# Kernel optimization log

Measured on AMD Instinct MI355X. Metric: run time of the kernel, lower is better.

Reference implementation:

```python
import jax, jax.numpy as jnp
import numpy as np

B, S, E, H, FFN = 4, 1024, 1024, 16, 4096
D = E // H
EPS = 1e-5


def setup_inputs() -> dict:
    key = jax.random.key(0)
    ks = jax.random.split(key, 13)
    n = lambda k, shp, sc=1.0: jax.random.normal(k, shp, jnp.float32) * sc
    return {
        "x": n(ks[0], (B, S, E)),
        "wq": n(ks[1], (E, E), E ** -0.5),
        "wk": n(ks[2], (E, E), E ** -0.5),
        "wv": n(ks[3], (E, E), E ** -0.5),
        "phase": n(ks[4], (H, D)),  # nn.Parameter(torch.randn(H, d_k))
        "ln1_g": jnp.ones((E,), jnp.float32),
        "ln1_b": jnp.zeros((E,), jnp.float32),
        "ln2_g": jnp.ones((E,), jnp.float32),
        "ln2_b": jnp.zeros((E,), jnp.float32),
        "w1": n(ks[5], (FFN, E), E ** -0.5),
        "b1": n(ks[6], (FFN,), 0.02),
        "w2": n(ks[7], (E, FFN), FFN ** -0.5),
        "b2": n(ks[8], (E,), 0.02),
    }


def _layer_norm(x, g, b):
    mu = jnp.mean(x, -1, keepdims=True)
    xc = x - mu
    var = jnp.mean(xc * xc, -1, keepdims=True)  # biased, like torch LayerNorm
    return xc * jax.lax.rsqrt(var + EPS) * g + b


def reference(x, wq, wk, wv, phase, ln1_g, ln1_b, ln2_g, ln2_b, w1, b1, w2, b2):
    b_, s_, e_ = x.shape

    def proj(w):  # torch Linear: x @ w.T, then split heads -> [B,H,S,D]
        return jnp.einsum("bse,fe->bsf", x, w).reshape(b_, s_, H, D).transpose(0, 2, 1, 3)

    q, k, v = proj(wq), proj(wk), proj(wv)
    ph = jnp.exp(1j * phase)[None, :, None, :]  # [1,H,1,D] complex64
    qc, kc, vc = q * ph, k * ph, v * ph
    # complex QK^T (note: plain transpose, NOT conjugate, per source)
    scores = jnp.einsum("bhsd,bhtd->bhst", qc, kc) / jnp.sqrt(jnp.float32(D))
    # complex softmax: exp(z)/sum exp(z), stabilized by max of real part
    m = jnp.max(scores.real, -1, keepdims=True)
    ez = jnp.exp(scores - m)
    attn = ez / jnp.sum(ez, -1, keepdims=True)
    out = jnp.einsum("bhst,bhtd->bhsd", attn, vc).real  # take real part to re-enter real pipeline
    out = out.transpose(0, 2, 1, 3).reshape(b_, s_, e_)
    x1 = _layer_norm(x + out, ln1_g, ln1_b)
    h = jax.nn.relu(jnp.einsum("bse,fe->bsf", x1, w1) + b1)
    ffn = jnp.einsum("bsf,ef->bse", h, w2) + b2
    return _layer_norm(x1 + ffn, ln2_g, ln2_b)
```

## Files before the change

kernel.cpp:

```cpp
#include <hip/hip_runtime.h>

typedef unsigned short u16;
typedef unsigned int u32;
typedef u16 u16x4 __attribute__((ext_vector_type(4)));
typedef u16 u16x8 __attribute__((ext_vector_type(8)));
typedef u32 u32x2 __attribute__((ext_vector_type(2)));
typedef u32 u32x4 __attribute__((ext_vector_type(4)));
typedef float f32x4 __attribute__((ext_vector_type(4)));
typedef __bf16 bf16x8 __attribute__((ext_vector_type(8)));

#define B_N 4
#define S_N 1024
#define E_N 1024
#define H_N 16
#define D_N 64
#define F_N 4096
#define NTOK 4096

#define SCK 0.18033688011112042f
#define SSK 0.01989436788648692f

static __device__ __forceinline__ u16 f2bf(float f) {
  u32 u = __builtin_bit_cast(u32, f);
  return (u16)((u + 0x7fffu + ((u >> 16) & 1u)) >> 16);
}
static __device__ __forceinline__ float bf2f(u16 v) {
  return __builtin_bit_cast(float, ((u32)v) << 16);
}
static __device__ __forceinline__ f32x4 mfma16(u16x8 a, u16x8 b, f32x4 c) {
  return __builtin_amdgcn_mfma_f32_16x16x32_bf16(
      __builtin_bit_cast(bf16x8, a), __builtin_bit_cast(bf16x8, b), c, 0, 0, 0);
}
static __device__ __forceinline__ float exp2_hw(float x) {
  float r; asm("v_exp_f32 %0, %1" : "=v"(r) : "v"(x)); return r;
}
static __device__ __forceinline__ float sin_hw(float x) {
  float r; asm("v_sin_f32 %0, %1" : "=v"(r) : "v"(x)); return r;
}
static __device__ __forceinline__ float cos_hw(float x) {
  float r; asm("v_cos_f32 %0, %1" : "=v"(r) : "v"(x)); return r;
}
static __device__ __forceinline__ u32 cvtpk(float lo, float hi) {
  u32 r; asm("v_cvt_pk_bf16_f32 %0, %1, %2" : "=v"(r) : "v"(lo), "v"(hi)); return r;
}
#define GLOAD16(gp, lp)                                              \
  __builtin_amdgcn_global_load_lds(                                  \
      (const __attribute__((address_space(1))) void*)(gp),           \
      (__attribute__((address_space(3))) void*)(lp), 16, 0, 0)

__global__ __launch_bounds__(256) void cvt_all(
    const float* __restrict__ s0, u16* __restrict__ d0, int n0,
    const float* __restrict__ s1, u16* __restrict__ d1, int n1,
    const float* __restrict__ s2, u16* __restrict__ d2, int n2,
    const float* __restrict__ s3, u16* __restrict__ d3, int n3,
    const float* __restrict__ s4, u16* __restrict__ d4, int n4,
    const float* __restrict__ s5, u16* __restrict__ d5, int n5) {
  const int seg = blockIdx.y;
  const float* src; u16* dst; int n;
  switch (seg) {
    case 0: src = s0; dst = d0; n = n0; break;
    case 1: src = s1; dst = d1; n = n1; break;
    case 2: src = s2; dst = d2; n = n2; break;
    case 3: src = s3; dst = d3; n = n3; break;
    case 4: src = s4; dst = d4; n = n4; break;
    default: src = s5; dst = d5; n = n5; break;
  }
  int i = blockIdx.x * 256 + threadIdx.x;
  if (i < n) {
    float4 v = ((const float4*)src)[i];
    u16x4 o;
    o[0] = f2bf(v.x); o[1] = f2bf(v.y); o[2] = f2bf(v.z); o[3] = f2bf(v.w);
    ((u16x4*)dst)[i] = o;
  }
}

template <int MODE, int KTILES>
__global__ __launch_bounds__(512, 4) void gemm2p(
    const u16* __restrict__ A, const u16* __restrict__ B0,
    const u16* __restrict__ B1, const u16* __restrict__ B2, int strideK,
    u16* __restrict__ o0, u16* __restrict__ o1, u16* __restrict__ o2,
    const float* __restrict__ biasp) {
  constexpr int BM = 128, BN = 128;
  constexpr int MR = BM / 32;
  constexpr int NR = BN / 64;
  constexpr int CA = BM / 64;
  constexpr int CB = BN / 64;
  constexpr int RS = BN * 2;
  constexpr int CM = BN / 8 - 1;
  constexpr int LCPR = 4;
  constexpr int RC = (BM * BN) / 4096;
  __shared__ u16 SMEM[(BM + BN) * 128];
  char* const base = (char*)SMEM;
  auto Abase = [&](int b) { return base + b * (BM * 128); };
  auto Bbase = [&](int b) { return base + 2 * (BM * 128) + b * (BN * 128); };

  const int tid = threadIdx.x;
  const int lane = tid & 63, wv = tid >> 6;
  const int l15 = lane & 15, l4 = lane >> 4;
  const int wr = wv >> 2, wc = wv & 3;

  int lin = blockIdx.x;
  { const int q = (int)gridDim.x >> 3; lin = (lin & 7) * q + (lin >> 3); }
  int bxr, by, kc = 0, region = 0;
  const u16* Bsrc = B0;
  if constexpr (MODE == 0) {
    const int bxa = lin % 24; by = lin / 24;
    region = bxa >> 3; bxr = bxa & 7;
    Bsrc = (region == 0) ? B0 : (region == 1) ? B1 : B2;
  } else if constexpr (MODE == 1) {
    bxr = lin & 31; by = lin >> 5;
  } else {
    bxr = lin & 7; by = (lin >> 3) & 31; kc = lin >> 8;
  }

  const u16* Ab = A + (size_t)(by * BM) * strideK + (size_t)kc * (KTILES * 64);
  const u16* Bb = Bsrc + (size_t)(bxr * BN) * strideK + (size_t)kc * (KTILES * 64);

  auto stage = [&](int buf, int kt) {
#pragma unroll
    for (int i = 0; i < CA; ++i) {
      const int c = (wv * CA + i) * 64 + lane;
      const int row = c >> 3, slot = (c & 7) ^ (row & 7);
      GLOAD16(Ab + (size_t)row * strideK + kt * 64 + slot * 8,
              Abase(buf) + (wv * CA + i) * 1024);
    }
#pragma unroll
    for (int i = 0; i < CB; ++i) {
      const int c = (wv * CB + i) * 64 + lane;
      const int row = c >> 3, slot = (c & 7) ^ (row & 7);
      GLOAD16(Bb + (size_t)row * strideK + kt * 64 + slot * 8,
              Bbase(buf) + (wv * CB + i) * 1024);
    }
  };

  f32x4 z4 = {0.f, 0.f, 0.f, 0.f};
  f32x4 acc[MR][NR];
#pragma unroll
  for (int m = 0; m < MR; ++m)
#pragma unroll
    for (int n = 0; n < NR; ++n) acc[m][n] = z4;

  stage(0, 0);
  __syncthreads();

  int buf = 0;
#pragma unroll 1
  for (int t = 0; t < KTILES; ++t) {
    if (t + 1 < KTILES) stage(buf ^ 1, t + 1);
#pragma unroll
    for (int kp = 0; kp < 2; ++kp) {
      u16x8 afr[MR], bfr[NR];
#pragma unroll
      for (int m = 0; m < MR; ++m) {
        const int row = wr * (BM / 2) + m * 16 + l15;
        const int off = row * 128 + ((((kp << 2) | l4) ^ (row & 7)) << 4);
        afr[m] = *(const u16x8*)(Abase(buf) + off);
      }
#pragma unroll
      for (int n = 0; n < NR; ++n) {
        const int row = wc * (BN / 4) + n * 16 + l15;
        const int off = row * 128 + ((((kp << 2) | l4) ^ (row & 7)) << 4);
        bfr[n] = *(const u16x8*)(Bbase(buf) + off);
      }
      __builtin_amdgcn_s_setprio(1);
#pragma unroll
      for (int m = 0; m < MR; ++m)
#pragma unroll
        for (int n = 0; n < NR; ++n) acc[m][n] = mfma16(afr[m], bfr[n], acc[m][n]);
      __builtin_amdgcn_s_setprio(0);
    }
    if (t + 1 < KTILES) {
      __syncthreads();
      buf ^= 1;
    }
  }

  __syncthreads();
  float bvv[NR];
  if constexpr (MODE == 1) {
#pragma unroll
    for (int n = 0; n < NR; ++n)
      bvv[n] = biasp[bxr * BN + wc * (BN / 4) + n * 16 + l15];
  }
  const bool vtile = (MODE == 0) && (region == 2);
#pragma unroll
  for (int n = 0; n < NR; ++n)
#pragma unroll
    for (int m = 0; m < MR; ++m)
#pragma unroll
      for (int j = 0; j < 4; ++j) {
        const int row = wr * (BM / 2) + m * 16 + l4 * 4 + j;
        const int col = wc * (BN / 4) + n * 16 + l15;
        float v = acc[m][n][j];
        if constexpr (MODE == 1) v = fmaxf(v + bvv[n], 0.f);
        const int fr = vtile ? col : row;
        const int fc = vtile ? row : col;
        *(u16*)(base + fr * RS + ((((fc >> 3) ^ (fr & CM))) << 4) +
                (fc & 7) * 2) = f2bf(v);
      }
  __syncthreads();
  if constexpr (MODE == 0) {
    if (region == 2) {
#pragma unroll
      for (int i = 0; i < RC; ++i) {
        const int q = i * 512 + tid;
        const int crow = q >> LCPR, slot = q & CM;
        const u16x8 v = *(const u16x8*)(base + crow * RS +
                                        ((slot ^ (crow & CM)) << 4));
        const int ch = bxr * BN + crow;
        const int hI = ch >> 6, dI = ch & 63;
        const int tok = by * BM + slot * 8;
        const int bI = tok >> 10, sI = tok & 1023;
        *(u16x8*)(o2 + (((size_t)(bI * H_N + hI)) * D_N + dI) * S_N + sI) = v;
      }
    } else {
      u16* outb = (region == 0) ? o0 : o1;
#pragma unroll
      for (int i = 0; i < RC; ++i) {
        const int q = i * 512 + tid;
        const int row = q >> LCPR, c = q & CM;
        const u16x8 v = *(const u16x8*)(base + row * RS +
                                        ((c ^ (row & CM)) << 4));
        const int gr = by * BM + row;
        const int gcol = bxr * BN + c * 8;
        const int bI = gr >> 10, sI = gr & 1023;
        const int hI = gcol >> 6, dI = gcol & 63;
        *(u16x8*)(outb + (((size_t)(bI * H_N + hI)) * S_N + sI) * D_N + dI) = v;
      }
    }
  } else if constexpr (MODE == 1) {
#pragma unroll
    for (int i = 0; i < RC; ++i) {
      const int q = i * 512 + tid;
      const int row = q >> LCPR, c = q & CM;
      const u16x8 v = *(const u16x8*)(base + row * RS + ((c ^ (row & CM)) << 4));
      *(u16x8*)(o0 + (size_t)(by * BM + row) * F_N + bxr * BN + c * 8) = v;
    }
  } else {
#pragma unroll
    for (int i = 0; i < RC; ++i) {
      const int q = i * 512 + tid;
      const int row = q >> LCPR, c = q & CM;
      const u16x8 v = *(const u16x8*)(base + row * RS + ((c ^ (row & CM)) << 4));
      const size_t gr = (size_t)kc * NTOK + by * BM + row;
      *(u16x8*)(o0 + gr * E_N + bxr * BN + c * 8) = v;
    }
  }
}

__global__ __launch_bounds__(512, 4) void attn_kernel(
    const u16* __restrict__ Qg, const u16* __restrict__ Kg,
    const u16* __restrict__ Vtg, const float* __restrict__ phase,
    u16* __restrict__ outp) {
  __shared__ u16 KS[64 * 64];
  __shared__ u16 VT[64 * 64];
  __shared__ u16 PreS[128 * 32], PimS[128 * 32];

  const int tid = threadIdx.x;
  const int lane = tid & 63, wv = tid >> 6;
  const int l15 = lane & 15, l4 = lane >> 4;
  const int L = blockIdx.x;
  const int within = L >> 3;
  const int qt = within & 7;
  const int g = (L & 7) * 8 + (within >> 3);
  const int hh = g & 15, bb = g >> 4;
  const size_t hoff = ((size_t)(bb * H_N + hh)) * (size_t)(S_N * D_N);
  const u16* K0 = Kg + hoff;
  const u16* Vt0 = Vtg + hoff;
  const int qrow = wv * 16 + l15;

  u16x8 qcf[2], qsf[2];
#pragma unroll
  for (int ks = 0; ks < 2; ++ks) {
    const u16x8 qraw = *(const u16x8*)(
        Qg + hoff + (size_t)(qt * 128 + qrow) * D_N + ks * 32 + l4 * 8);
#pragma unroll
    for (int e = 0; e < 8; ++e) {
      const int d = ks * 32 + l4 * 8 + e;
      float sp, cp;
      __sincosf(2.f * phase[hh * 64 + d], &sp, &cp);
      const float qv = bf2f(qraw[e]);
      qcf[ks][e] = f2bf(qv * cp * SCK);
      qsf[ks][e] = f2bf(qv * sp * SSK);
    }
  }

  f32x4 z4 = {0.f, 0.f, 0.f, 0.f};
  f32x4 U1[4], U2[4];
#pragma unroll
  for (int db = 0; db < 4; ++db) { U1[db] = z4; U2[db] = z4; }
  float zre = 0.f, zim = 0.f;

  const int krow = tid >> 3, kslot = tid & 7;
  const int loff = (krow * 128 + kslot * 16) ^ ((krow & 7) << 4);

  u32x4 rk = *(const u32x4*)(K0 + (size_t)krow * 64 + kslot * 8);
  u32x4 rv = *(const u32x4*)(Vt0 + (size_t)krow * S_N + kslot * 8);

  for (int kt = 0; kt < 16; ++kt) {
    *(u32x4*)((char*)KS + loff) = rk;
    *(u32x4*)((char*)VT + loff) = rv;
    if (kt < 15) {
      rk = *(const u32x4*)(K0 + (size_t)((kt + 1) * 64 + krow) * 64 + kslot * 8);
      rv = *(const u32x4*)(Vt0 + (size_t)krow * S_N + (kt + 1) * 64 + kslot * 8);
    }
    __syncthreads();

#pragma unroll
    for (int ts = 0; ts < 2; ++ts) {
      f32x4 sre[2], sim[2];
      sre[0] = z4; sre[1] = z4; sim[0] = z4; sim[1] = z4;
      __builtin_amdgcn_s_setprio(1);
#pragma unroll
      for (int tb = 0; tb < 2; ++tb) {
        const int trow = ts * 32 + tb * 16 + l15;
#pragma unroll
        for (int ks = 0; ks < 2; ++ks) {
          const int off = trow * 128 + ((((ks << 2) | l4) ^ (trow & 7)) << 4);
          u16x8 ak = *(const u16x8*)((const char*)KS + off);
          sre[tb] = mfma16(ak, qcf[ks], sre[tb]);
          sim[tb] = mfma16(ak, qsf[ks], sim[tb]);
        }
      }
      __builtin_amdgcn_s_setprio(0);

#pragma unroll
      for (int tb = 0; tb < 2; ++tb) {
        float pc[4], ps[4];
#pragma unroll
        for (int j = 0; j < 4; ++j) {
          const float e = exp2_hw(sre[tb][j]);
          const float sn = sin_hw(sim[tb][j]);
          const float cs = cos_hw(sim[tb][j]);
          pc[j] = e * cs; ps[j] = e * sn;
        }
        zre += (pc[0] + pc[1]) + (pc[2] + pc[3]);
        zim += (ps[0] + ps[1]) + (ps[2] + ps[3]);
        u32x2 wre = {cvtpk(pc[0], pc[1]), cvtpk(pc[2], pc[3])};
        u32x2 wim = {cvtpk(ps[0], ps[1]), cvtpk(ps[2], ps[3])};
        const int offp = (qrow * 64 + tb * 32 + l4 * 8) ^ (((qrow >> 1) & 3) << 4);
        *(u32x2*)((char*)PreS + offp) = wre;
        *(u32x2*)((char*)PimS + offp) = wim;
      }

      const int offp2 = (qrow * 64 + (l4 << 4)) ^ (((qrow >> 1) & 3) << 4);
      u16x8 bre = *(const u16x8*)((const char*)PreS + offp2);
      u16x8 bim = *(const u16x8*)((const char*)PimS + offp2);
      __builtin_amdgcn_s_setprio(1);
#pragma unroll
      for (int db = 0; db < 4; ++db) {
        const int dd = db * 16 + l15;
        const int offv = dd * 128 + ((((ts << 2) | l4) ^ (dd & 7)) << 4);
        u16x8 av = *(const u16x8*)((const char*)VT + offv);
        U1[db] = mfma16(av, bre, U1[db]);
        U2[db] = mfma16(av, bim, U2[db]);
      }
      __builtin_amdgcn_s_setprio(0);
    }
    __syncthreads();
  }

  float zr = zre, zi = zim;
  zr += __shfl_xor(zr, 16); zr += __shfl_xor(zr, 32);
  zi += __shfl_xor(zi, 16); zi += __shfl_xor(zi, 32);
  const float inv = 1.f / (zr * zr + zi * zi);
  const int q = qt * 128 + qrow;
  u16* orow = outp + ((size_t)(bb * S_N + q)) * E_N + hh * 64;
#pragma unroll
  for (int db = 0; db < 4; ++db) {
    float o[4];
#pragma unroll
    for (int j = 0; j < 4; ++j) {
      const int d = db * 16 + l4 * 4 + j;
      float sp, cp;
      __sincosf(phase[hh * 64 + d], &sp, &cp);
      const float nre = cp * U1[db][j] - sp * U2[db][j];
      const float nim = sp * U1[db][j] + cp * U2[db][j];
      o[j] = (nre * zr + nim * zi) * inv;
    }
    u32x2 w = {cvtpk(o[0], o[1]), cvtpk(o[2], o[3])};
    *(u32x2*)(orow + db * 16 + l4 * 4) = w;
  }
}

__global__ __launch_bounds__(256) void add_ln_kernel(
    const float* __restrict__ a, const u16* __restrict__ r,
    const float* __restrict__ g, const float* __restrict__ be,
    u16* __restrict__ outb) {
  const int tid = threadIdx.x;
  const int row = blockIdx.x;
  const int lane = tid & 63, wv = tid >> 6;
  const float4 va = ((const float4*)(a + (size_t)row * 1024))[tid];
  const u16x4 rr = *(const u16x4*)(r + (size_t)row * 1024 + tid * 4);
  float4 v;
  v.x = va.x + bf2f(rr[0]); v.y = va.y + bf2f(rr[1]);
  v.z = va.z + bf2f(rr[2]); v.w = va.w + bf2f(rr[3]);
  float s = v.x + v.y + v.z + v.w;
#pragma unroll
  for (int m = 1; m < 64; m <<= 1) s += __shfl_xor(s, m);
  __shared__ float red[8];
  if (lane == 0) red[wv] = s;
  __syncthreads();
  s = red[0] + red[1] + red[2] + red[3];
  const float mu = s * (1.f / 1024.f);
  float4 xc;
  xc.x = v.x - mu; xc.y = v.y - mu; xc.z = v.z - mu; xc.w = v.w - mu;
  float q = xc.x * xc.x + xc.y * xc.y + xc.z * xc.z + xc.w * xc.w;
#pragma unroll
  for (int m = 1; m < 64; m <<= 1) q += __shfl_xor(q, m);
  if (lane == 0) red[4 + wv] = q;
  __syncthreads();
  q = red[4] + red[5] + red[6] + red[7];
  const float rs = rsqrtf(q * (1.f / 1024.f) + 1e-5f);
  const float4 gg = ((const float4*)g)[tid];
  const float4 bb4 = ((const float4*)be)[tid];
  u16x4 ob;
  ob[0] = f2bf(xc.x * rs * gg.x + bb4.x);
  ob[1] = f2bf(xc.y * rs * gg.y + bb4.y);
  ob[2] = f2bf(xc.z * rs * gg.z + bb4.z);
  ob[3] = f2bf(xc.w * rs * gg.w + bb4.w);
  *(u16x4*)(outb + (size_t)row * 1024 + tid * 4) = ob;
}

__global__ __launch_bounds__(256) void add_ln4_kernel(
    const u16* __restrict__ part,
    const u16* __restrict__ resid,
    const float* __restrict__ bias,
    const float* __restrict__ g, const float* __restrict__ be,
    float* __restrict__ outp) {
  const int tid = threadIdx.x;
  const int row = blockIdx.x;
  const int lane = tid & 63, wv = tid >> 6;
  const float4 bv = ((const float4*)bias)[tid];
  float4 v = {bv.x, bv.y, bv.z, bv.w};
#pragma unroll
  for (int kc = 0; kc < 2; ++kc) {
    const u16x4 pp = *(const u16x4*)(part + ((size_t)kc * NTOK + row) * 1024 + tid * 4);
    v.x += bf2f(pp[0]); v.y += bf2f(pp[1]); v.z += bf2f(pp[2]); v.w += bf2f(pp[3]);
  }
  const u16x4 rr = *(const u16x4*)(resid + (size_t)row * 1024 + tid * 4);
  v.x += bf2f(rr[0]); v.y += bf2f(rr[1]); v.z += bf2f(rr[2]); v.w += bf2f(rr[3]);
  float s = v.x + v.y + v.z + v.w;
#pragma unroll
  for (int m = 1; m < 64; m <<= 1) s += __shfl_xor(s, m);
  __shared__ float red[8];
  if (lane == 0) red[wv] = s;
  __syncthreads();
  s = red[0] + red[1] + red[2] + red[3];
  const float mu = s * (1.f / 1024.f);
  float4 xc;
  xc.x = v.x - mu; xc.y = v.y - mu; xc.z = v.z - mu; xc.w = v.w - mu;
  float q = xc.x * xc.x + xc.y * xc.y + xc.z * xc.z + xc.w * xc.w;
#pragma unroll
  for (int m = 1; m < 64; m <<= 1) q += __shfl_xor(q, m);
  if (lane == 0) red[4 + wv] = q;
  __syncthreads();
  q = red[4] + red[5] + red[6] + red[7];
  const float rs = rsqrtf(q * (1.f / 1024.f) + 1e-5f);
  const float4 gg = ((const float4*)g)[tid];
  const float4 bb4 = ((const float4*)be)[tid];
  float4 o;
  o.x = xc.x * rs * gg.x + bb4.x;
  o.y = xc.y * rs * gg.y + bb4.y;
  o.z = xc.z * rs * gg.z + bb4.z;
  o.w = xc.w * rs * gg.w + bb4.w;
  ((float4*)(outp + (size_t)row * 1024))[tid] = o;
}

extern "C" void kernel_launch(void* const* d_in, const int* in_sizes, int n_in,
                              void* d_out, int out_size, void* d_ws, size_t ws_size,
                              hipStream_t stream) {
  (void)in_sizes; (void)n_in; (void)out_size; (void)ws_size;
  const float* x = (const float*)d_in[0];
  const float* wq = (const float*)d_in[1];
  const float* wk = (const float*)d_in[2];
  const float* wvp = (const float*)d_in[3];
  const float* phase = (const float*)d_in[4];
  const float* ln1g = (const float*)d_in[5];
  const float* ln1b = (const float*)d_in[6];
  const float* ln2g = (const float*)d_in[7];
  const float* ln2b = (const float*)d_in[8];
  const float* w1 = (const float*)d_in[9];
  const float* b1 = (const float*)d_in[10];
  const float* w2 = (const float*)d_in[11];
  const float* b2 = (const float*)d_in[12];
  float* outp = (float*)d_out;

  char* p = (char*)d_ws;
  auto alloc = [&](size_t n) -> char* {
    char* q = p;
    p += (n + 255) & ~(size_t)255;
    return q;
  };
  const size_t TOKE = (size_t)NTOK * E_N;
  u16* xb = (u16*)alloc(TOKE * 2);
  u16* wqb = (u16*)alloc((size_t)E_N * E_N * 2);
  u16* wkb = (u16*)alloc((size_t)E_N * E_N * 2);
  u16* wvb = (u16*)alloc((size_t)E_N * E_N * 2);
  u16* w1b = (u16*)alloc((size_t)F_N * E_N * 2);
  u16* w2b = (u16*)alloc((size_t)E_N * F_N * 2);
  u16* Qp  = (u16*)alloc(TOKE * 2);
  u16* pad = (u16*)alloc(TOKE * 2);
  u16* Kp  = (u16*)alloc(TOKE * 2);
  u16* Vtp = (u16*)alloc(TOKE * 2);
  u16* sp0 = (u16*)alloc(TOKE * 2);
  u16* attn_o = (u16*)alloc(TOKE * 4);
  alloc(TOKE * 2);
  (void)pad;
  u16* x1b = xb;
  u16* hb = Qp;
  u16* part = sp0;

  dim3 blk(256);
  cvt_all<<<dim3(4096, 6), blk, 0, stream>>>(
      x, xb, (int)(TOKE / 4),
      wq, wqb, E_N * E_N / 4,
      wk, wkb, E_N * E_N / 4,
      wvp, wvb, E_N * E_N / 4,
      w1, w1b, F_N * E_N / 4,
      w2, w2b, E_N * F_N / 4);

  gemm2p<0, 16><<<dim3(768), dim3(512), 0, stream>>>(
      xb, wqb, wkb, wvb, E_N, Qp, Kp, Vtp, nullptr);

  attn_kernel<<<dim3(512), dim3(512), 0, stream>>>(
      Qp, Kp, Vtp, phase, attn_o);

  add_ln_kernel<<<dim3(NTOK), blk, 0, stream>>>(x, attn_o, ln1g, ln1b, x1b);

  gemm2p<1, 16><<<dim3(1024), dim3(512), 0, stream>>>(
      x1b, w1b, nullptr, nullptr, E_N, hb, nullptr, nullptr, b1);

  gemm2p<2, 32><<<dim3(512), dim3(512), 0, stream>>>(
      hb, w2b, nullptr, nullptr, F_N, part, nullptr, nullptr, nullptr);

  add_ln4_kernel<<<dim3(NTOK), blk, 0, stream>>>(part, x1b, b2, ln2g, ln2b, outp);
}
```

Measured before the change: 178.5 us.

## Split attention key loop across two wave groups with LDS reduction

The attention kernel now launches 1024 threads per block as two groups of eight waves. Each group processes half of the key/value tiles in its own LDS buffers, and the partial accumulators and normalizer sums are then reduced through shared memory before group 0 writes the output. The aim is to double the waves resident per CU and halve the serial key-loop length, to better hide latency. The cost is a 64KB LDS footprint, an extra reduction epilogue, and tighter register limits from the new launch bounds, which could cause spilling.

```diff
diff --git a/kernel.cpp b/kernel.cpp
--- a/kernel.cpp
+++ b/kernel.cpp
@@ -248,17 +248,23 @@
   }
 }
 
-__global__ __launch_bounds__(512, 4) void attn_kernel(
+__global__ __launch_bounds__(1024, 8) void attn_kernel(
     const u16* __restrict__ Qg, const u16* __restrict__ Kg,
     const u16* __restrict__ Vtg, const float* __restrict__ phase,
     u16* __restrict__ outp) {
-  __shared__ u16 KS[64 * 64];
-  __shared__ u16 VT[64 * 64];
-  __shared__ u16 PreS[128 * 32], PimS[128 * 32];
+  __shared__ u16 SMEM[32768];
+  char* const base = (char*)SMEM;
 
   const int tid = threadIdx.x;
   const int lane = tid & 63, wv = tid >> 6;
+  const int grp = wv >> 3, wg = wv & 7;
+  const int tid_g = tid & 511;
   const int l15 = lane & 15, l4 = lane >> 4;
+  char* const KSb = base + grp * 8192;
+  char* const VTb = base + 16384 + grp * 8192;
+  char* const Preb = base + 32768 + grp * 8192;
+  char* const Pimb = base + 49152 + grp * 8192;
+
   const int L = blockIdx.x;
   const int within = L >> 3;
   const int qt = within & 7;
@@ -267,7 +273,7 @@
   const size_t hoff = ((size_t)(bb * H_N + hh)) * (size_t)(S_N * D_N);
   const u16* K0 = Kg + hoff;
   const u16* Vt0 = Vtg + hoff;
-  const int qrow = wv * 16 + l15;
+  const int qrow = wg * 16 + l15;
 
   u16x8 qcf[2], qsf[2];
 #pragma unroll
@@ -291,18 +297,19 @@
   for (int db = 0; db < 4; ++db) { U1[db] = z4; U2[db] = z4; }
   float zre = 0.f, zim = 0.f;
 
-  const int krow = tid >> 3, kslot = tid & 7;
+  const int krow = tid_g >> 3, kslot = tid_g & 7;
   const int loff = (krow * 128 + kslot * 16) ^ ((krow & 7) << 4);
-
-  u32x4 rk = *(const u32x4*)(K0 + (size_t)krow * 64 + kslot * 8);
-  u32x4 rv = *(const u32x4*)(Vt0 + (size_t)krow * S_N + kslot * 8);
-
-  for (int kt = 0; kt < 16; ++kt) {
-    *(u32x4*)((char*)KS + loff) = rk;
-    *(u32x4*)((char*)VT + loff) = rv;
-    if (kt < 15) {
-      rk = *(const u32x4*)(K0 + (size_t)((kt + 1) * 64 + krow) * 64 + kslot * 8);
-      rv = *(const u32x4*)(Vt0 + (size_t)krow * S_N + (kt + 1) * 64 + kslot * 8);
+  const int tbase = grp * 8;
+
+  u32x4 rk = *(const u32x4*)(K0 + (size_t)(tbase * 64 + krow) * 64 + kslot * 8);
+  u32x4 rv = *(const u32x4*)(Vt0 + (size_t)krow * S_N + tbase * 64 + kslot * 8);
+
+  for (int kt = 0; kt < 8; ++kt) {
+    *(u32x4*)(KSb + loff) = rk;
+    *(u32x4*)(VTb + loff) = rv;
+    if (kt < 7) {
+      rk = *(const u32x4*)(K0 + (size_t)((tbase + kt + 1) * 64 + krow) * 64 + kslot * 8);
+      rv = *(const u32x4*)(Vt0 + (size_t)krow * S_N + (tbase + kt + 1) * 64 + kslot * 8);
     }
     __syncthreads();
 
@@ -317,7 +324,7 @@
 #pragma unroll
         for (int ks = 0; ks < 2; ++ks) {
           const int off = trow * 128 + ((((ks << 2) | l4) ^ (trow & 7)) << 4);
-          u16x8 ak = *(const u16x8*)((const char*)KS + off);
+          u16x8 ak = *(const u16x8*)(KSb + off);
           sre[tb] = mfma16(ak, qcf[ks], sre[tb]);
           sim[tb] = mfma16(ak, qsf[ks], sim[tb]);
         }
@@ -339,19 +346,19 @@
         u32x2 wre = {cvtpk(pc[0], pc[1]), cvtpk(pc[2], pc[3])};
         u32x2 wim = {cvtpk(ps[0], ps[1]), cvtpk(ps[2], ps[3])};
         const int offp = (qrow * 64 + tb * 32 + l4 * 8) ^ (((qrow >> 1) & 3) << 4);
-        *(u32x2*)((char*)PreS + offp) = wre;
-        *(u32x2*)((char*)PimS + offp) = wim;
+        *(u32x2*)(Preb + offp) = wre;
+        *(u32x2*)(Pimb + offp) = wim;
       }
 
       const int offp2 = (qrow * 64 + (l4 << 4)) ^ (((qrow >> 1) & 3) << 4);
-      u16x8 bre = *(const u16x8*)((const char*)PreS + offp2);
-      u16x8 bim = *(const u16x8*)((const char*)PimS + offp2);
+      u16x8 bre = *(const u16x8*)(Preb + offp2);
+      u16x8 bim = *(const u16x8*)(Pimb + offp2);
       __builtin_amdgcn_s_setprio(1);
 #pragma unroll
       for (int db = 0; db < 4; ++db) {
         const int dd = db * 16 + l15;
         const int offv = dd * 128 + ((((ts << 2) | l4) ^ (dd & 7)) << 4);
-        u16x8 av = *(const u16x8*)((const char*)VT + offv);
+        u16x8 av = *(const u16x8*)(VTb + offv);
         U1[db] = mfma16(av, bre, U1[db]);
         U2[db] = mfma16(av, bim, U2[db]);
       }
@@ -363,23 +370,56 @@
   float zr = zre, zi = zim;
   zr += __shfl_xor(zr, 16); zr += __shfl_xor(zr, 32);
   zi += __shfl_xor(zi, 16); zi += __shfl_xor(zi, 32);
-  const float inv = 1.f / (zr * zr + zi * zi);
-  const int q = qt * 128 + qrow;
-  u16* orow = outp + ((size_t)(bb * S_N + q)) * E_N + hh * 64;
-#pragma unroll
-  for (int db = 0; db < 4; ++db) {
-    float o[4];
-#pragma unroll
-    for (int j = 0; j < 4; ++j) {
-      const int d = db * 16 + l4 * 4 + j;
-      float sp, cp;
-      __sincosf(phase[hh * 64 + d], &sp, &cp);
-      const float nre = cp * U1[db][j] - sp * U2[db][j];
-      const float nim = sp * U1[db][j] + cp * U2[db][j];
-      o[j] = (nre * zr + nim * zi) * inv;
-    }
-    u32x2 w = {cvtpk(o[0], o[1]), cvtpk(o[2], o[3])};
-    *(u32x2*)(orow + db * 16 + l4 * 4) = w;
+
+  float* zbuf = (float*)base;
+  if (grp == 1 && l4 == 0) {
+    zbuf[qrow * 2] = zr;
+    zbuf[qrow * 2 + 1] = zi;
+  }
+  __syncthreads();
+  if (grp == 0) {
+    zr += zbuf[qrow * 2];
+    zi += zbuf[qrow * 2 + 1];
+  }
+  __syncthreads();
+
+  float* ubuf = (float*)base;
+  if (grp == 1) {
+#pragma unroll
+    for (int db = 0; db < 4; ++db)
+#pragma unroll
+      for (int j = 0; j < 4; ++j) {
+        ubuf[(db * 4 + j) * 512 + tid_g] = U1[db][j];
+        ubuf[(16 + db * 4 + j) * 512 + tid_g] = U2[db][j];
+      }
+  }
+  __syncthreads();
+  if (grp == 0) {
+#pragma unroll
+    for (int db = 0; db < 4; ++db)
+#pragma unroll
+      for (int j = 0; j < 4; ++j) {
+        U1[db][j] += ubuf[(db * 4 + j) * 512 + tid_g];
+        U2[db][j] += ubuf[(16 + db * 4 + j) * 512 + tid_g];
+      }
+    const float inv = 1.f / (zr * zr + zi * zi);
+    const int q = qt * 128 + qrow;
+    u16* orow = outp + ((size_t)(bb * S_N + q)) * E_N + hh * 64;
+#pragma unroll
+    for (int db = 0; db < 4; ++db) {
+      float o[4];
+#pragma unroll
+      for (int j = 0; j < 4; ++j) {
+        const int d = db * 16 + l4 * 4 + j;
+        float sp, cp;
+        __sincosf(phase[hh * 64 + d], &sp, &cp);
+        const float nre = cp * U1[db][j] - sp * U2[db][j];
+        const float nim = sp * U1[db][j] + cp * U2[db][j];
+        o[j] = (nre * zr + nim * zi) * inv;
+      }
+      u32x2 w = {cvtpk(o[0], o[1]), cvtpk(o[2], o[3])};
+      *(u32x2*)(orow + db * 16 + l4 * 4) = w;
+    }
   }
 }
 
@@ -523,7 +563,7 @@
   gemm2p<0, 16><<<dim3(768), dim3(512), 0, stream>>>(
       xb, wqb, wkb, wvb, E_N, Qp, Kp, Vtp, nullptr);
 
-  attn_kernel<<<dim3(512), dim3(512), 0, stream>>>(
+  attn_kernel<<<dim3(512), dim3(1024), 0, stream>>>(
       Qp, Kp, Vtp, phase, attn_o);
 
   add_ln_kernel<<<dim3(NTOK), blk, 0, stream>>>(x, attn_o, ln1g, ln1b, x1b);
```

New measurement: 450.6 us. +152.4%, slower.
